# Kernel tuning notes

Hardware: AMD Instinct MI355X
Metric: run time of the kernel (lower is better)

The kernel has to match this reference:

```python
import jax, jax.numpy as jnp
import numpy as np

NH, NP = 8, 4  # n_heads, n_points
SHAPES = [(100, 167), (50, 84), (25, 42), (13, 21)]  # (H, W) per level


def setup_inputs() -> dict:
    key = jax.random.key(0)
    ks = jax.random.split(key, 8)
    bs, dm = 2, 256
    nl = len(SHAPES)
    nv = sum(h * w for h, w in SHAPES)  # 22223
    nq = nv
    s = 1.0 / np.sqrt(dm)
    return {
        'query': jax.random.normal(ks[0], (bs, nq, dm), jnp.float32),
        'value': jax.random.normal(ks[1], (bs, nv, dm), jnp.float32),
        'reference_points': jax.random.uniform(ks[2], (bs, nq, nl, 2), jnp.float32),
        'W_so': jax.random.normal(ks[3], (dm, NH * nl * NP * 2), jnp.float32) * 0.01,
        'b_so': jax.random.normal(ks[4], (NH * nl * NP * 2,), jnp.float32) * 0.5,
        'W_aw': jax.random.normal(ks[5], (dm, NH * nl * NP), jnp.float32) * s,
        'b_aw': jnp.zeros((NH * nl * NP,), jnp.float32),
        'W_vp': jax.random.normal(ks[6], (dm, dm), jnp.float32) * s,
        'b_vp': jnp.zeros((dm,), jnp.float32),
        'W_op': jax.random.normal(ks[7], (dm, dm), jnp.float32) * s,
        'b_op': jnp.zeros((dm,), jnp.float32),
        'spatial_shapes': jnp.array(SHAPES, jnp.int32),
    }


def _bilinear_gather(vf, H, W, loc):
    # vf: [BH, H*W, dh] flattened level feature map; loc: [BH, QP, 2] in [0,1]
    # Matches torch grid_sample(mode='bilinear', padding_mode='zeros', align_corners=False)
    x = loc[..., 0] * W - 0.5
    y = loc[..., 1] * H - 0.5
    x0f = jnp.floor(x); y0f = jnp.floor(y)
    lx = x - x0f; ly = y - y0f
    x0 = x0f.astype(jnp.int32); y0 = y0f.astype(jnp.int32)
    out = jnp.zeros(vf.shape[:1] + loc.shape[1:2] + vf.shape[-1:], vf.dtype)
    for dx, dy, w in ((0, 0, (1 - lx) * (1 - ly)), (1, 0, lx * (1 - ly)),
                      (0, 1, (1 - lx) * ly), (1, 1, lx * ly)):
        xi = x0 + dx; yi = y0 + dy
        valid = (xi >= 0) & (xi < W) & (yi >= 0) & (yi < H)
        idx = jnp.clip(yi, 0, H - 1) * W + jnp.clip(xi, 0, W - 1)  # [BH, QP]
        g = jnp.take_along_axis(vf, idx[:, :, None], axis=1)  # [BH, QP, dh]
        out = out + g * (w * valid)[:, :, None]
    return out


def _msda(value_heads, shapes_np, loc, aw):
    # value_heads: [bs,nv,nh,dh], loc: [bs,nq,nh,nl,np,2], aw: [bs,nq,nh,nl,np]
    bs, nv, nh, dh = value_heads.shape
    nq, nl, npnt = loc.shape[1], loc.shape[3], loc.shape[4]
    out = jnp.zeros((bs * nh, nq, dh), value_heads.dtype)
    start = 0
    for lvl in range(nl):
        H, W = int(shapes_np[lvl, 0]), int(shapes_np[lvl, 1])
        vf = value_heads[:, start:start + H * W].transpose(0, 2, 1, 3).reshape(bs * nh, H * W, dh)
        loc_l = loc[:, :, :, lvl].transpose(0, 2, 1, 3, 4).reshape(bs * nh, nq * npnt, 2)
        samp = _bilinear_gather(vf, H, W, loc_l).reshape(bs * nh, nq, npnt, dh)
        aw_l = aw[:, :, :, lvl].transpose(0, 2, 1, 3).reshape(bs * nh, nq, npnt)
        out = out + jnp.einsum('bqpd,bqp->bqd', samp, aw_l)
        start += H * W
    return out.reshape(bs, nh, nq, dh).transpose(0, 2, 1, 3).reshape(bs, nq, nh * dh)


def reference(query, value, reference_points, W_so, b_so, W_aw, b_aw, W_vp, b_vp, W_op, b_op, spatial_shapes):
    bs, nq, dm = query.shape
    nl = reference_points.shape[2]
    dh = dm // NH
    v = (value @ W_vp + b_vp).reshape(bs, value.shape[1], NH, dh)
    off = (query @ W_so + b_so).reshape(bs, nq, NH, nl, NP, 2)
    aw = jax.nn.softmax((query @ W_aw + b_aw).reshape(bs, nq, NH, nl * NP), axis=-1)
    aw = aw.reshape(bs, nq, NH, nl, NP)
    ss = np.asarray(spatial_shapes)  # static level metadata
    normalizer = jnp.asarray(np.stack([ss[:, 1], ss[:, 0]], -1), query.dtype)  # (w, h) per level
    loc = reference_points[:, :, None, :, None, :] + off / normalizer[None, None, None, :, None, :]
    out = _msda(v, ss, loc, aw)
    return out @ W_op + b_op + query  # identity residual (identity defaults to query)
```

## Files before the change

### kernel.cpp

```cpp
#include <hip/hip_runtime.h>
#include <hip/hip_bf16.h>
#include <math.h>

typedef __hip_bfloat16 bf16;
using f32x4  = __attribute__((ext_vector_type(4))) float;
using f32x2  = __attribute__((ext_vector_type(2))) float;
using bf16x8 = __attribute__((ext_vector_type(8))) short;
using f16x2  = __attribute__((ext_vector_type(2))) _Float16;

constexpr int BS = 2, NQ = 22223, MROWS = 44446;
constexpr int LH[4] = {100, 50, 25, 13};
constexpr int LW[4] = {167, 84, 42, 21};
constexpr int LSTART[4] = {0, 16700, 20900, 21950};
constexpr int PLW[4] = {170, 87, 45, 24};
constexpr int PLSTART[4] = {0, 17510, 22121, 23381};
constexpr int PTOT = 23765;

constexpr int BM = 128, BK = 32;
constexpr int LDT = 40;
constexpr int GX = (MROWS + BM - 1) / BM;

__global__ __launch_bounds__(256) void prep_weights(
    const float* __restrict__ W_vp, const float* __restrict__ W_so,
    const float* __restrict__ W_aw, const float* __restrict__ W_op,
    const float* __restrict__ b_so, const float* __restrict__ b_aw,
    bf16* __restrict__ Wt_vp, bf16* __restrict__ Wt_cat,
    bf16* __restrict__ Wt_op, float* __restrict__ bcat)
{
    int i = blockIdx.x * 256 + threadIdx.x;
    if (i < 256 * 256) {
        int n = i >> 8, k = i & 255;
        Wt_vp[i] = __float2bfloat16(W_vp[k * 256 + n]);
        Wt_op[i] = __float2bfloat16(W_op[k * 256 + n]);
    }
    if (i < 384 * 256) {
        int n = i >> 8, k = i & 255;
        float v = (n < 256) ? W_so[k * 256 + n] : W_aw[k * 128 + (n - 256)];
        Wt_cat[i] = __float2bfloat16(v);
    }
    if (i < 384) bcat[i] = (i < 256) ? b_so[i] : b_aw[i - 256];
}

__device__ inline int pad_row_idx(int r) {
    int b = 0, pix = r;
    if (pix >= NQ) { b = 1; pix -= NQ; }
    int base;
    if (pix < LSTART[1])      { int rel = pix;             int y = rel / 167; int x = rel - y * 167; base = PLSTART[0] + (y + 1) * 170 + (x + 1); }
    else if (pix < LSTART[2]) { int rel = pix - LSTART[1]; int y = rel / 84;  int x = rel - y * 84;  base = PLSTART[1] + (y + 1) * 87  + (x + 1); }
    else if (pix < LSTART[3]) { int rel = pix - LSTART[2]; int y = rel / 42;  int x = rel - y * 42;  base = PLSTART[2] + (y + 1) * 45  + (x + 1); }
    else                      { int rel = pix - LSTART[3]; int y = rel / 21;  int x = rel - y * 21;  base = PLSTART[3] + (y + 1) * 24  + (x + 1); }
    return b * PTOT + base;
}

template<bool A_BF16>
__device__ __forceinline__ void mfma_core(
    const void* __restrict__ Av, int lda, const bf16* __restrict__ Wt,
    int row0, int bn0, int M, bf16* As, bf16* Bs, f32x4 (&acc)[4][4])
{
    const int tid = threadIdx.x;
    const int lane = tid & 63;
    const int wv = tid >> 6;
    const int wm = (wv >> 1) * 64, wn = (wv & 1) * 64;
    const int l15 = lane & 15, l4 = lane >> 4;

#pragma unroll
    for (int m = 0; m < 4; ++m)
#pragma unroll
        for (int n = 0; n < 4; ++n) { acc[m][n][0]=0.f; acc[m][n][1]=0.f; acc[m][n][2]=0.f; acc[m][n][3]=0.f; }

    for (int k0 = 0; k0 < 256; k0 += BK) {
        __syncthreads();
#pragma unroll
        for (int t = 0; t < 2; ++t) {
            int idx = tid + t * 256;
            int r = idx >> 2, s = idx & 3;
            {
                int grow = row0 + r; if (grow >= M) grow = M - 1;
                bf16 tmp[8];
                if constexpr (A_BF16) {
                    const bf16* ap = (const bf16*)Av + (size_t)grow * lda + (k0 + s * 8);
                    *(uint4*)tmp = *(const uint4*)ap;
                } else {
                    const float* ap = (const float*)Av + (size_t)grow * lda + (k0 + s * 8);
                    f32x4 v0 = *(const f32x4*)ap;
                    f32x4 v1 = *(const f32x4*)(ap + 4);
#pragma unroll
                    for (int j = 0; j < 4; ++j) tmp[j] = __float2bfloat16(v0[j]);
#pragma unroll
                    for (int j = 0; j < 4; ++j) tmp[4 + j] = __float2bfloat16(v1[j]);
                }
                *(uint4*)&As[r * LDT + s * 8] = *(const uint4*)tmp;
            }
            *(uint4*)&Bs[r * LDT + s * 8] =
                *(const uint4*)(Wt + (size_t)(bn0 + r) * 256 + (k0 + s * 8));
        }
        __syncthreads();

        bf16x8 af[4], bfr[4];
#pragma unroll
        for (int m = 0; m < 4; ++m)
            af[m] = *(const bf16x8*)&As[(wm + m * 16 + l15) * LDT + l4 * 8];
#pragma unroll
        for (int n = 0; n < 4; ++n)
            bfr[n] = *(const bf16x8*)&Bs[(wn + n * 16 + l15) * LDT + l4 * 8];
#pragma unroll
        for (int m = 0; m < 4; ++m)
#pragma unroll
            for (int n = 0; n < 4; ++n)
                acc[m][n] = __builtin_amdgcn_mfma_f32_16x16x32_bf16(af[m], bfr[n], acc[m][n], 0, 0, 0);
    }
}

__global__ __launch_bounds__(256) void gemm_producer(
    const float* __restrict__ query, const float* __restrict__ value,
    const bf16* __restrict__ Wt_cat, const bf16* __restrict__ Wt_vp,
    const float* __restrict__ bcat, const float* __restrict__ bvp,
    bf16* __restrict__ offawl, _Float16* __restrict__ vproj)
{
    __shared__ bf16 As[BM * LDT];
    __shared__ bf16 Bs[BM * LDT];

    constexpr int NWG = GX * 5;
    constexpr int QXW = NWG / 8, RXW = NWG % 8;
    int orig = blockIdx.x;
    int xcd = orig & 7, seq = orig >> 3;
    int swz = (xcd < RXW ? xcd * (QXW + 1) : RXW * (QXW + 1) + (xcd - RXW) * QXW) + seq;
    int slice = swz % 5;
    int row0 = (swz / 5) * BM;

    const bool isOff = slice < 3;
    const void* A = isOff ? (const void*)query : (const void*)value;
    const bf16* Wt = isOff ? Wt_cat : Wt_vp;
    const float* bias = isOff ? bcat : bvp;
    int bn0 = isOff ? slice * 128 : (slice - 3) * 128;

    f32x4 acc[4][4];
    mfma_core<false>(A, 256, Wt, row0, bn0, MROWS, As, Bs, acc);

    const int lane = threadIdx.x & 63;
    const int wv = threadIdx.x >> 6;
    const int wm = (wv >> 1) * 64, wn = (wv & 1) * 64;
    const int l15 = lane & 15, l4 = lane >> 4;

    if (isOff) {
#pragma unroll
        for (int m = 0; m < 4; ++m)
#pragma unroll
            for (int j = 0; j < 4; ++j) {
                int r = row0 + wm + m * 16 + l4 * 4 + j;
                if (r < MROWS) {
                    bf16* orow = offawl + (size_t)r * 384;
#pragma unroll
                    for (int n = 0; n < 4; ++n) {
                        int fcol = bn0 + wn + n * 16 + l15;
                        orow[fcol] = __float2bfloat16(acc[m][n][j] + bias[fcol]);
                    }
                }
            }
    } else {
#pragma unroll
        for (int m = 0; m < 4; ++m)
#pragma unroll
            for (int j = 0; j < 4; ++j) {
                int r = row0 + wm + m * 16 + l4 * 4 + j;
                if (r < MROWS) {
                    _Float16* orow = vproj + (size_t)pad_row_idx(r) * 256;
#pragma unroll
                    for (int n = 0; n < 4; ++n) {
                        int fcol = bn0 + wn + n * 16 + l15;
                        orow[fcol] = (_Float16)(acc[m][n][j] + bias[fcol]);
                    }
                }
            }
    }
}

__global__ __launch_bounds__(256) void gemm_out(
    const bf16* __restrict__ msda, const bf16* __restrict__ Wt_op,
    const float* __restrict__ b_op, const float* __restrict__ query,
    float* __restrict__ out)
{
    __shared__ bf16 As[BM * LDT];
    __shared__ bf16 Bs[BM * LDT];

    constexpr int NWG = GX * 2;
    int orig = blockIdx.x;
    int swz = (orig & 7) * (NWG / 8) + (orig >> 3);
    int bn0 = (swz & 1) * 128;
    int row0 = (swz >> 1) * BM;

    f32x4 acc[4][4];
    mfma_core<true>(msda, 384, Wt_op, row0, bn0, MROWS, As, Bs, acc);

    const int lane = threadIdx.x & 63;
    const int wv = threadIdx.x >> 6;
    const int wm = (wv >> 1) * 64, wn = (wv & 1) * 64;
    const int l15 = lane & 15, l4 = lane >> 4;

#pragma unroll
    for (int m = 0; m < 4; ++m)
#pragma unroll
        for (int j = 0; j < 4; ++j) {
            int r = row0 + wm + m * 16 + l4 * 4 + j;
            if (r < MROWS) {
#pragma unroll
                for (int n = 0; n < 4; ++n) {
                    int fcol = bn0 + wn + n * 16 + l15;
                    out[(size_t)r * 256 + fcol] =
                        acc[m][n][j] + b_op[fcol] + query[(size_t)r * 256 + fcol];
                }
            }
        }
}

__device__ inline f32x2 bfpair(unsigned u) {
    f32x2 r;
    r.x = __uint_as_float(u << 16);
    r.y = __uint_as_float(u & 0xffff0000u);
    return r;
}

__global__ __launch_bounds__(256, 4) void msda_sample8(
    const _Float16* __restrict__ vproj,
    const bf16* __restrict__ offawl,
    const float* __restrict__ refp,
    bf16* __restrict__ msda_out)
{
    __shared__ uint2 sOA[8][128];
    __shared__ float sRef[8][8];

    constexpr int NBLK = (MROWS + 7) / 8;
    constexpr int QX = NBLK / 8, RX = NBLK % 8;
    const int orig = blockIdx.x;
    const int xcd = orig & 7, seq = orig >> 3;
    const int blk = (xcd < RX ? xcd * (QX + 1) : RX * (QX + 1) + (xcd - RX) * QX) + seq;
    const int q0 = blk * 8;

    const int tid = threadIdx.x;

#pragma unroll
    for (int k = 0; k < 4; ++k) {
        int idx = tid + k * 256;
        int row = idx >> 7, e = idx & 127;
        if (e < 96) {
            int grow = min(q0 + row, MROWS - 1);
            sOA[row][e] = *((const uint2*)(offawl + (size_t)grow * 384) + e);
        }
    }
    if (tid < 64) {
        int row = tid >> 3, er = tid & 7;
        int grow = min(q0 + row, MROWS - 1);
        sRef[row][er] = refp[(size_t)grow * 8 + er];
    }
    __syncthreads();

    const int w = tid >> 6;
    const int lane = tid & 63;
    const int qs = lane >> 5;
    const int h = (lane >> 2) & 7;
    const int s = lane & 3;
    const int qrow = w * 2 + qs;
    int q = q0 + qrow;
    const bool alive = q < MROWS;
    if (!alive) q = MROWS - 1;
    const int b = (q >= NQ) ? 1 : 0;

    const char* rowp = (const char*)&sOA[qrow][0];
    unsigned off16[16];
    {
        uint4 o0 = *(const uint4*)(rowp + h * 64);
        uint4 o1 = *(const uint4*)(rowp + h * 64 + 16);
        uint4 o2 = *(const uint4*)(rowp + h * 64 + 32);
        uint4 o3 = *(const uint4*)(rowp + h * 64 + 48);
        off16[0]=o0.x; off16[1]=o0.y; off16[2]=o0.z; off16[3]=o0.w;
        off16[4]=o1.x; off16[5]=o1.y; off16[6]=o1.z; off16[7]=o1.w;
        off16[8]=o2.x; off16[9]=o2.y; off16[10]=o2.z; off16[11]=o2.w;
        off16[12]=o3.x; off16[13]=o3.y; off16[14]=o3.z; off16[15]=o3.w;
    }

    float aw[16];
    {
        uint4 g0 = *(const uint4*)(rowp + 512 + h * 32);
        uint4 g1 = *(const uint4*)(rowp + 512 + h * 32 + 16);
        unsigned gu[8] = {g0.x,g0.y,g0.z,g0.w,g1.x,g1.y,g1.z,g1.w};
        float lg[16];
#pragma unroll
        for (int i = 0; i < 8; ++i) {
            f32x2 p = bfpair(gu[i]);
            lg[2*i] = p.x; lg[2*i+1] = p.y;
        }
        float mx = lg[0];
#pragma unroll
        for (int i = 1; i < 16; ++i) mx = fmaxf(mx, lg[i]);
        float ssum = 0.f;
#pragma unroll
        for (int i = 0; i < 16; ++i) { aw[i] = __expf(lg[i] - mx); ssum += aw[i]; }
        float inv = 1.f / ssum;
#pragma unroll
        for (int i = 0; i < 16; ++i) aw[i] *= inv;
    }

    f16x2 acc0 = {0, 0}, acc1 = {0, 0}, acc2 = {0, 0}, acc3 = {0, 0};

#pragma unroll
    for (int l = 0; l < 4; ++l) {
        const int W = LW[l], H = LH[l], Wp = PLW[l];
        const float xb = sRef[qrow][l * 2 + 0] * (float)W + 0.5f;
        const float yb = sRef[qrow][l * 2 + 1] * (float)H + 0.5f;
        const _Float16* vl = vproj + ((size_t)(b * PTOT + PLSTART[l])) * 256 + h * 32 + s * 8;

        const _Float16* p00[4];
        f16x2 hw[4][4];
#pragma unroll
        for (int p = 0; p < 4; ++p) {
            const int t = l * 4 + p;
            f32x2 o2 = bfpair(off16[t]);
            float x = fminf(fmaxf(xb + o2.x, 0.f), (float)(W + 1));
            float y = fminf(fmaxf(yb + o2.y, 0.f), (float)(H + 1));
            float x0f = floorf(x), y0f = floorf(y);
            float lx = x - x0f, ly = y - y0f;
            int x0 = (int)x0f, y0 = (int)y0f;
            p00[p] = vl + (size_t)((y0 * Wp + x0) * 256);
            float aww = aw[t];
            float wx0 = 1.f - lx;
            float wy0 = (1.f - ly) * aww, wy1 = ly * aww;
            _Float16 h00 = (_Float16)(wx0 * wy0), h01 = (_Float16)(lx * wy0);
            _Float16 h10 = (_Float16)(wx0 * wy1), h11 = (_Float16)(lx * wy1);
            hw[p][0] = f16x2{h00, h00}; hw[p][1] = f16x2{h01, h01};
            hw[p][2] = f16x2{h10, h10}; hw[p][3] = f16x2{h11, h11};
        }

        uint4 c[4][4];
#pragma unroll
        for (int p = 0; p < 4; ++p) {
            c[p][0] = *(const uint4*)(p00[p]);
            c[p][1] = *(const uint4*)(p00[p] + 256);
            c[p][2] = *(const uint4*)(p00[p] + Wp * 256);
            c[p][3] = *(const uint4*)(p00[p] + Wp * 256 + 256);
        }

#pragma unroll
        for (int p = 0; p < 4; ++p)
#pragma unroll
            for (int cc = 0; cc < 4; ++cc) {
                acc0 += __builtin_bit_cast(f16x2, c[p][cc].x) * hw[p][cc];
                acc1 += __builtin_bit_cast(f16x2, c[p][cc].y) * hw[p][cc];
                acc2 += __builtin_bit_cast(f16x2, c[p][cc].z) * hw[p][cc];
                acc3 += __builtin_bit_cast(f16x2, c[p][cc].w) * hw[p][cc];
            }
    }

    if (alive) {
        bf16 ob[8];
        ob[0] = __float2bfloat16((float)acc0[0]);
        ob[1] = __float2bfloat16((float)acc0[1]);
        ob[2] = __float2bfloat16((float)acc1[0]);
        ob[3] = __float2bfloat16((float)acc1[1]);
        ob[4] = __float2bfloat16((float)acc2[0]);
        ob[5] = __float2bfloat16((float)acc2[1]);
        ob[6] = __float2bfloat16((float)acc3[0]);
        ob[7] = __float2bfloat16((float)acc3[1]);
        *(uint4*)(msda_out + (size_t)q * 384 + h * 32 + s * 8) = *(const uint4*)ob;
    }
}

extern "C" void kernel_launch(void* const* d_in, const int* in_sizes, int n_in,
                              void* d_out, int out_size, void* d_ws, size_t ws_size,
                              hipStream_t stream) {
    const float* query = (const float*)d_in[0];
    const float* value = (const float*)d_in[1];
    const float* refp  = (const float*)d_in[2];
    const float* W_so  = (const float*)d_in[3];
    const float* b_so  = (const float*)d_in[4];
    const float* W_aw  = (const float*)d_in[5];
    const float* b_aw  = (const float*)d_in[6];
    const float* W_vp  = (const float*)d_in[7];
    const float* b_vp  = (const float*)d_in[8];
    const float* W_op  = (const float*)d_in[9];
    const float* b_op  = (const float*)d_in[10];
    float* out = (float*)d_out;

    bf16*     d_offawl = (bf16*)d_ws;
    _Float16* d_vproj  = (_Float16*)(d_offawl + (size_t)MROWS * 384);
    bf16*     d_wtcat  = (bf16*)(d_vproj + (size_t)2 * PTOT * 256);
    bf16*     d_wtvp   = d_wtcat + 384 * 256;
    bf16*     d_wtop   = d_wtvp + 256 * 256;
    float*    d_bcat   = (float*)(d_wtop + 256 * 256);

    prep_weights<<<384, 256, 0, stream>>>(W_vp, W_so, W_aw, W_op, b_so, b_aw,
                                          d_wtvp, d_wtcat, d_wtop, d_bcat);
    hipMemsetAsync(d_vproj, 0, (size_t)2 * PTOT * 256 * sizeof(_Float16), stream);

    gemm_producer<<<GX * 5, 256, 0, stream>>>(
        query, value, d_wtcat, d_wtvp, d_bcat, b_vp, d_offawl, d_vproj);

    msda_sample8<<<(MROWS + 7) / 8, 256, 0, stream>>>(
        d_vproj, d_offawl, refp, d_offawl);

    gemm_out<<<GX * 2, 256, 0, stream>>>(d_offawl, d_wtop, b_op, query, out);
}
```

Before: 170.2 us.

## Store projected values head-major so bilinear gathers hit compact per-head planes

```diff
diff --git a/kernel.cpp b/kernel.cpp
--- a/kernel.cpp
+++ b/kernel.cpp
@@ -41,15 +41,11 @@
     if (i < 384) bcat[i] = (i < 256) ? b_so[i] : b_aw[i - 256];
 }
 
-__device__ inline int pad_row_idx(int r) {
-    int b = 0, pix = r;
-    if (pix >= NQ) { b = 1; pix -= NQ; }
-    int base;
-    if (pix < LSTART[1])      { int rel = pix;             int y = rel / 167; int x = rel - y * 167; base = PLSTART[0] + (y + 1) * 170 + (x + 1); }
-    else if (pix < LSTART[2]) { int rel = pix - LSTART[1]; int y = rel / 84;  int x = rel - y * 84;  base = PLSTART[1] + (y + 1) * 87  + (x + 1); }
-    else if (pix < LSTART[3]) { int rel = pix - LSTART[2]; int y = rel / 42;  int x = rel - y * 42;  base = PLSTART[2] + (y + 1) * 45  + (x + 1); }
-    else                      { int rel = pix - LSTART[3]; int y = rel / 21;  int x = rel - y * 21;  base = PLSTART[3] + (y + 1) * 24  + (x + 1); }
-    return b * PTOT + base;
+__device__ inline int pad_base_idx(int pix) {
+    if (pix < LSTART[1])      { int y = pix / 167;                  int x = pix - y * 167;                return PLSTART[0] + (y + 1) * 170 + (x + 1); }
+    else if (pix < LSTART[2]) { int rel = pix - LSTART[1]; int y = rel / 84; int x = rel - y * 84;        return PLSTART[1] + (y + 1) * 87  + (x + 1); }
+    else if (pix < LSTART[3]) { int rel = pix - LSTART[2]; int y = rel / 42; int x = rel - y * 42;        return PLSTART[2] + (y + 1) * 45  + (x + 1); }
+    else                      { int rel = pix - LSTART[3]; int y = rel / 21; int x = rel - y * 21;        return PLSTART[3] + (y + 1) * 24  + (x + 1); }
 }
 
 template<bool A_BF16>
@@ -164,11 +160,14 @@
             for (int j = 0; j < 4; ++j) {
                 int r = row0 + wm + m * 16 + l4 * 4 + j;
                 if (r < MROWS) {
-                    _Float16* orow = vproj + (size_t)pad_row_idx(r) * 256;
+                    int bb = (r >= NQ) ? 1 : 0;
+                    int pb = pad_base_idx(r - bb * NQ);
 #pragma unroll
                     for (int n = 0; n < 4; ++n) {
                         int fcol = bn0 + wn + n * 16 + l15;
-                        orow[fcol] = (_Float16)(acc[m][n][j] + bias[fcol]);
+                        int hh = fcol >> 5, cc = fcol & 31;
+                        vproj[((size_t)(hh * 2 + bb) * PTOT + pb) * 32 + cc] =
+                            (_Float16)(acc[m][n][j] + bias[fcol]);
                     }
                 }
             }
@@ -220,7 +219,9 @@
     return r;
 }
 
-__global__ __launch_bounds__(256, 4) void msda_sample8(
+__global__ __launch_bounds__(256)
+__attribute__((amdgpu_waves_per_eu(2, 4)))
+void msda_sample10(
     const _Float16* __restrict__ vproj,
     const bf16* __restrict__ offawl,
     const float* __restrict__ refp,
@@ -307,9 +308,9 @@
         const int W = LW[l], H = LH[l], Wp = PLW[l];
         const float xb = sRef[qrow][l * 2 + 0] * (float)W + 0.5f;
         const float yb = sRef[qrow][l * 2 + 1] * (float)H + 0.5f;
-        const _Float16* vl = vproj + ((size_t)(b * PTOT + PLSTART[l])) * 256 + h * 32 + s * 8;
-
-        const _Float16* p00[4];
+        const _Float16* vl = vproj + ((size_t)(h * 2 + b) * PTOT + PLSTART[l]) * 32 + s * 8;
+
+        const _Float16* pp[4];
         f16x2 hw[4][4];
 #pragma unroll
         for (int p = 0; p < 4; ++p) {
@@ -320,7 +321,7 @@
             float x0f = floorf(x), y0f = floorf(y);
             float lx = x - x0f, ly = y - y0f;
             int x0 = (int)x0f, y0 = (int)y0f;
-            p00[p] = vl + (size_t)((y0 * Wp + x0) * 256);
+            pp[p] = vl + (size_t)((y0 * Wp + x0) * 32);
             float aww = aw[t];
             float wx0 = 1.f - lx;
             float wy0 = (1.f - ly) * aww, wy1 = ly * aww;
@@ -333,10 +334,10 @@
         uint4 c[4][4];
 #pragma unroll
         for (int p = 0; p < 4; ++p) {
-            c[p][0] = *(const uint4*)(p00[p]);
-            c[p][1] = *(const uint4*)(p00[p] + 256);
-            c[p][2] = *(const uint4*)(p00[p] + Wp * 256);
-            c[p][3] = *(const uint4*)(p00[p] + Wp * 256 + 256);
+            c[p][0] = *(const uint4*)(pp[p]);
+            c[p][1] = *(const uint4*)(pp[p] + 32);
+            c[p][2] = *(const uint4*)(pp[p] + Wp * 32);
+            c[p][3] = *(const uint4*)(pp[p] + Wp * 32 + 32);
         }
 
 #pragma unroll
@@ -382,19 +383,19 @@
 
     bf16*     d_offawl = (bf16*)d_ws;
     _Float16* d_vproj  = (_Float16*)(d_offawl + (size_t)MROWS * 384);
-    bf16*     d_wtcat  = (bf16*)(d_vproj + (size_t)2 * PTOT * 256);
+    bf16*     d_wtcat  = (bf16*)(d_vproj + (size_t)16 * PTOT * 32);
     bf16*     d_wtvp   = d_wtcat + 384 * 256;
     bf16*     d_wtop   = d_wtvp + 256 * 256;
     float*    d_bcat   = (float*)(d_wtop + 256 * 256);
 
     prep_weights<<<384, 256, 0, stream>>>(W_vp, W_so, W_aw, W_op, b_so, b_aw,
                                           d_wtvp, d_wtcat, d_wtop, d_bcat);
-    hipMemsetAsync(d_vproj, 0, (size_t)2 * PTOT * 256 * sizeof(_Float16), stream);
+    hipMemsetAsync(d_vproj, 0, (size_t)16 * PTOT * 32 * sizeof(_Float16), stream);
 
     gemm_producer<<<GX * 5, 256, 0, stream>>>(
         query, value, d_wtcat, d_wtvp, d_bcat, b_vp, d_offawl, d_vproj);
 
-    msda_sample8<<<(MROWS + 7) / 8, 256, 0, stream>>>(
+    msda_sample10<<<(MROWS + 7) / 8, 256, 0, stream>>>(
         d_vproj, d_offawl, refp, d_offawl);
 
     gemm_out<<<GX * 2, 256, 0, stream>>>(d_offawl, d_wtop, b_op, query, out);
```

Result: faster. 164.3 us (-3.5%).
